# Kernel optimization log

Hardware: AMD Instinct MI355X
Metric: run time of the kernel (lower is better)

The kernel has to match this reference:

```python
import jax, jax.numpy as jnp
import numpy as np

N = 100000   # nodes
E = 1600000  # edges
H = 128      # hidden_dim
B = 4096     # number of root pairs
HOPS = 3


def setup_inputs() -> dict:
    key = jax.random.key(0)
    ks = jax.random.split(key, 12)
    s = 0.05
    return {
        "node_feat": jax.random.normal(ks[0], (N, H), jnp.float32),
        "send_embd": jax.random.normal(ks[1], (N, H), jnp.float32),
        "edge_index": jax.random.randint(ks[2], (2, E), 0, N, dtype=jnp.int32),
        "root_index": jax.random.randint(ks[3], (2 * B,), 0, N, dtype=jnp.int32),
        "agg_by_source": 1,
        "lin1_W": jax.random.normal(ks[4], (2 * H, H), jnp.float32) * s,
        "lin1_b": jnp.zeros((H,), jnp.float32),
        "gat_W": jax.random.normal(ks[5], (HOPS, H, H), jnp.float32) * s,
        "gat_asrc": jax.random.normal(ks[6], (HOPS, H), jnp.float32) * s,
        "gat_adst": jax.random.normal(ks[7], (HOPS, H), jnp.float32) * s,
        "gat_b": jnp.zeros((HOPS, H), jnp.float32),
        "lstm_Wih": jax.random.normal(ks[8], (HOPS, 2 * H, 4 * H), jnp.float32) * s,
        "lstm_Whh": jax.random.normal(ks[9], (HOPS, H, 4 * H), jnp.float32) * s,
        "lstm_b": jnp.zeros((HOPS, 4 * H), jnp.float32),
        "lin2_W": jax.random.normal(ks[10], (H, H), jnp.float32) * s,
        "lin2_b": jnp.zeros((H,), jnp.float32),
    }


def _gat_breadth(x, src, dst, W, a_src, a_dst, b):
    # GATConv(heads=1) followed by tanh (GeniePath Breadth layer)
    xw = x @ W                                  # [N, H]
    e_score = jax.nn.leaky_relu((xw @ a_src)[src] + (xw @ a_dst)[dst], 0.2)  # [E]
    # softmax over incoming edges of each destination node
    m = jax.ops.segment_max(e_score, dst, num_segments=N)
    ex = jnp.exp(e_score - m[dst])
    z = jax.ops.segment_sum(ex, dst, num_segments=N)
    alpha = ex / z[dst]                          # [E]
    agg = jax.ops.segment_sum(alpha[:, None] * xw[src], dst, num_segments=N)
    return jnp.tanh(agg + b)


def _lstm_step(inp, h, c, Wih, Whh, b):
    gates = inp @ Wih + h @ Whh + b              # [N, 4H]
    i, f, g, o = jnp.split(gates, 4, axis=-1)
    c = jax.nn.sigmoid(f) * c + jax.nn.sigmoid(i) * jnp.tanh(g)
    h = jax.nn.sigmoid(o) * jnp.tanh(c)
    return h, c


def reference(node_feat, send_embd, edge_index, root_index, agg_by_source,
              lin1_W, lin1_b, gat_W, gat_asrc, gat_adst, gat_b,
              lstm_Wih, lstm_Whh, lstm_b, lin2_W, lin2_b):
    src, dst = edge_index[0], edge_index[1]
    # Aggregation stage input: concat node embedding with broadcast embedding
    x = jnp.concatenate([node_feat, send_embd], axis=1) @ lin1_W + lin1_b  # [N, H]
    # GeniePathLazy: all breadth (GAT) layers run on the projected input x
    h_tmps = [
        _gat_breadth(x, src, dst, gat_W[i], gat_asrc[i], gat_adst[i], gat_b[i])
        for i in range(HOPS)
    ]
    # Depth: per-node LSTM over the hop axis, input = cat(h_tmp, x_prev)
    h = jnp.zeros_like(x)
    c = jnp.zeros_like(x)
    xs = x
    for i in range(HOPS):
        inp = jnp.concatenate([h_tmps[i], xs], axis=1)   # [N, 2H]
        h, c = _lstm_step(inp, h, c, lstm_Wih[i], lstm_Whh[i], lstm_b[i])
        xs = h
    out = xs @ lin2_W + lin2_b                            # [N, H]
    roots = root_index.reshape(-1, 2)
    src_nodes = roots[:, 0] if agg_by_source else roots[:, 1]
    return out[src_nodes]                                 # [B, H]
```

## Files before the change

kernel.cpp:

```cpp
#include <hip/hip_runtime.h>

constexpr int N  = 100000;
constexpr int E  = 1600000;
constexpr int H  = 128;
constexpr int NB = 4096;
constexpr int HOPS = 3;

constexpr int WOFF_L1  = 0;
constexpr int WOFF_GAT = 32768;
constexpr int WOFF_CAT = 81920;
constexpr int WOFF_L2  = 671744;
constexpr int WTOT     = 688128;

constexpr size_t ALIGN = 256;
constexpr size_t alup(size_t x) { return (x + ALIGN - 1) & ~(ALIGN - 1); }

constexpr size_t OFF_X       = 0;
constexpr size_t OFF_SSRC    = alup(OFF_X + (size_t)N * H * 4);
constexpr size_t OFF_SDST    = alup(OFF_SSRC + (size_t)3 * N * 4);
constexpr size_t OFF_WVEC    = alup(OFF_SDST + (size_t)3 * N * 4);
constexpr size_t OFF_SELMAP  = alup(OFF_WVEC + 6 * H * 4);
constexpr size_t OFF_NODELST = alup(OFF_SELMAP + (size_t)N * 4);
constexpr size_t OFF_CNT     = alup(OFF_NODELST + NB * 4);
constexpr size_t OFF_DEG     = alup(OFF_CNT + 256);
constexpr size_t OFF_OFFS    = alup(OFF_DEG + NB * 4);
constexpr size_t OFF_CURSOR  = alup(OFF_OFFS + (NB + 1) * 4);
constexpr size_t OFF_ESORT   = alup(OFF_CURSOR + NB * 4);
constexpr size_t OFF_AGGXH   = alup(OFF_ESORT + (size_t)E * 4);
constexpr size_t OFF_AGGXL   = alup(OFF_AGGXH + (size_t)3 * NB * H * 2);
constexpr size_t OFF_XSH     = alup(OFF_AGGXL + (size_t)3 * NB * H * 2);
constexpr size_t OFF_XSL     = alup(OFF_XSH + (size_t)NB * H * 2);
constexpr size_t OFF_HH      = alup(OFF_XSL + (size_t)NB * H * 2);
constexpr size_t OFF_HL      = alup(OFF_HH + (size_t)NB * H * 2);
constexpr size_t OFF_CBUF    = alup(OFF_HL + (size_t)NB * H * 2);
constexpr size_t OFF_L2OUT   = alup(OFF_CBUF + (size_t)NB * H * 4);
constexpr size_t OFF_WHI     = alup(OFF_L2OUT + (size_t)NB * H * 4);
constexpr size_t OFF_WLO     = alup(OFF_WHI + (size_t)WTOT * 2);

__device__ __forceinline__ float lrelu(float v) { return v > 0.f ? v : 0.2f * v; }
__device__ __forceinline__ float sigmoidf_(float v) { return 1.f / (1.f + __expf(-v)); }

__device__ __forceinline__ unsigned short f2bf(float f) {
  unsigned u = __float_as_uint(f);
  unsigned r = (u + 0x7FFFu + ((u >> 16) & 1u)) >> 16;
  return (unsigned short)r;
}
__device__ __forceinline__ float bf2f(unsigned short h) {
  return __uint_as_float((unsigned)h << 16);
}
__device__ __forceinline__ void split_rne(float f, unsigned short& hi, unsigned short& lo) {
// ... 4 lines not shown
__device__ __forceinline__ void split_trunc(float f, short* hi, short* lo) {
  unsigned u = __float_as_uint(f);
  *hi = (short)(u >> 16);
  float r = f - __uint_as_float(u & 0xFFFF0000u);
  *lo = (short)(__float_as_uint(r) >> 16);
}

typedef short bf16x8 __attribute__((ext_vector_type(8)));
typedef float f32x4  __attribute__((ext_vector_type(4)));

#define MFMA3(ACC, AH, AL, BH, BL)                                               \
  ACC = __builtin_amdgcn_mfma_f32_16x16x32_bf16(AH, BH, ACC, 0, 0, 0);           \
  ACC = __builtin_amdgcn_mfma_f32_16x16x32_bf16(AH, BL, ACC, 0, 0, 0);           \
  ACC = __builtin_amdgcn_mfma_f32_16x16x32_bf16(AL, BH, ACC, 0, 0, 0);

__global__ void init_ws(int* __restrict__ sel_map, int* __restrict__ deg,
                        int* __restrict__ cursor, int* __restrict__ cnt,
                        float* __restrict__ cbuf, unsigned short* __restrict__ hh,
                        unsigned short* __restrict__ hl) {
  int i = blockIdx.x * 256 + threadIdx.x;
  int stride = gridDim.x * 256;
  for (int n = i; n < N; n += stride) sel_map[n] = -1;
  for (int n = i; n < NB; n += stride) { deg[n] = 0; cursor[n] = 0; }
  if (i < 64) cnt[i] = 0;
  for (int n = i; n < NB * H; n += stride) { cbuf[n] = 0.f; hh[n] = 0; hl[n] = 0; }
}

__global__ void prep_kernel(const float* __restrict__ gat_W,
                            const float* __restrict__ a_src,
                            const float* __restrict__ a_dst,
                            float* __restrict__ wvec,
                            const float* __restrict__ lin1_W,
                            const float* __restrict__ Wih,
                            const float* __restrict__ Whh,
                            const float* __restrict__ lin2_W,
                            unsigned short* __restrict__ whi,
                            unsigned short* __restrict__ wlo) {
  if (blockIdx.x < 6) {
    int i = blockIdx.x >> 1, which = blockIdx.x & 1;
    int k = threadIdx.x;
    __shared__ float av[H];
    if (k < H) av[k] = which ? a_dst[i * H + k] : a_src[i * H + k];
    __syncthreads();
    if (k >= H) return;
    const float* Wr = gat_W + (size_t)i * H * H + (size_t)k * H;
    float s = 0.f;
    #pragma unroll 8
    for (int j = 0; j < H; j++) s = fmaf(Wr[j], av[j], s);
    wvec[(i * 2 + which) * H + k] = s;
    return;
  }
  int idx = (blockIdx.x - 6) * 256 + threadIdx.x;
  if (idx >= WTOT) return;
  float v;
  if (idx < WOFF_GAT) {
    int rel = idx;
    int e = rel & 7, lane = (rel >> 3) & 63, tile = rel >> 9;
    int nl = lane & 15, quad = lane >> 4;
    int c = tile & 7, t = tile >> 3;
    int n = c * 16 + nl, k = t * 32 + quad * 8 + e;
    v = lin1_W[k * 128 + n];
  } else if (idx < WOFF_CAT) {
    int rel = idx - WOFF_GAT;
    int hop = rel / 16384; rel %= 16384;
    int e = rel & 7, lane = (rel >> 3) & 63, tile = rel >> 9;
    int nl = lane & 15, quad = lane >> 4;
    int c = tile & 7, t = tile >> 3;
    int n = c * 16 + nl, k = t * 32 + quad * 8 + e;
    v = gat_W[hop * 16384 + k * 128 + n];
  } else if (idx < WOFF_L2) {
    int rel = idx - WOFF_CAT;
    int hop = rel / 196608; rel %= 196608;
    int e = rel & 7, lane = (rel >> 3) & 63, tile = rel >> 9;
    int nl = lane & 15, quad = lane >> 4;
    int c = tile & 31, t = tile >> 5;
    int ftile = c >> 2, g = c & 3;
    int col = g * 128 + ftile * 16 + nl;
    int k = t * 32 + quad * 8 + e;
    v = (k < 256) ? Wih[hop * 131072 + k * 512 + col]
                  : Whh[hop * 65536 + (k - 256) * 512 + col];
  } else {
    int rel = idx - WOFF_L2;
    int e = rel & 7, lane = (rel >> 3) & 63, tile = rel >> 9;
    int nl = lane & 15, quad = lane >> 4;
    int c = tile & 7, t = tile >> 3;
    int n = c * 16 + nl, k = t * 32 + quad * 8 + e;
    v = lin2_W[k * 128 + n];
  }
  unsigned short hh, ll;
  split_rne(v, hh, ll);
  whi[idx] = hh;
  wlo[idx] = ll;
}

__global__ void roots_assign(const int* __restrict__ root, const int* __restrict__ aggp,
                             int* __restrict__ sel_map, int* __restrict__ node_list,
                             int* __restrict__ cnt) {
  int b = blockIdx.x * 256 + threadIdx.x;
  if (b >= NB) return;
  int node = root[2 * b + (aggp[0] ? 0 : 1)];
  int old = atomicCAS(&sel_map[node], -1, -2);
  if (old == -1) {
    int c = atomicAdd(cnt, 1);
    sel_map[node] = c;
    node_list[c] = node;
  }
}

__global__ __launch_bounds__(256)
void gemm_lin1(const float* __restrict__ a0, const float* __restrict__ a1,
               const unsigned short* __restrict__ Bth,
               const unsigned short* __restrict__ Btl,
               const float* __restrict__ bias, float* __restrict__ Cc,
               const float* __restrict__ wvec,
               float* __restrict__ s_src, float* __restrict__ s_dst, int M) {
  const int t = threadIdx.x, lane = t & 63, wave = t >> 6;
  const int nl = lane & 15, quad = lane >> 4;
  const int rt = blockIdx.x * 128 + wave * 32;

  f32x4 acc[2][8];
  #pragma unroll
  for (int i = 0; i < 2; i++)
    #pragma unroll
    for (int c = 0; c < 8; c++) acc[i][c] = (f32x4){0.f, 0.f, 0.f, 0.f};

  #pragma unroll
  for (int kt = 0; kt < 8; kt++) {
    const float* A = (kt < 4) ? a0 : a1;
    const int kk = (kt & 3) * 32 + quad * 8;
    bf16x8 ahi[2], alo[2];
    #pragma unroll
    for (int i = 0; i < 2; i++) {
      int row = rt + i * 16 + nl;
      float4 v0 = make_float4(0.f, 0.f, 0.f, 0.f), v1 = v0;
      if (row < M) {
        const float* p = A + (size_t)row * H + kk;
        v0 = *(const float4*)p;
        v1 = *(const float4*)(p + 4);
      }
      float af[8] = {v0.x, v0.y, v0.z, v0.w, v1.x, v1.y, v1.z, v1.w};
      #pragma unroll
      for (int j = 0; j < 8; j++) {
        short h_, l_;
        split_trunc(af[j], &h_, &l_);
        ahi[i][j] = h_;
        alo[i][j] = l_;
      }
    }
    #pragma unroll
    for (int c = 0; c < 8; c++) {
      size_t boff = ((size_t)(kt * 8 + c) * 64 + lane) * 8;
      bf16x8 bh = *(const bf16x8*)(Bth + boff);
      bf16x8 bl = *(const bf16x8*)(Btl + boff);
      #pragma unroll
      for (int i = 0; i < 2; i++) { MFMA3(acc[i][c], ahi[i], alo[i], bh, bl); }
    }
  }

  float bv[8], wvf[6][8];
  #pragma unroll
  for (int c = 0; c < 8; c++) {
    int col = c * 16 + nl;
    bv[c] = bias[col];
    #pragma unroll
    for (int v6 = 0; v6 < 6; v6++) wvf[v6][c] = wvec[v6 * 128 + col];
  }
  #pragma unroll
  for (int i = 0; i < 2; i++)
    #pragma unroll
    for (int r = 0; r < 4; r++) {
      int row = rt + i * 16 + quad * 4 + r;
      if (row >= M) continue;
      float* cr = Cc + (size_t)row * H;
      float sc[6] = {0.f, 0.f, 0.f, 0.f, 0.f, 0.f};
      #pragma unroll
      for (int c = 0; c < 8; c++) {
        float val = acc[i][c][r] + bv[c];
        cr[c * 16 + nl] = val;
        #pragma unroll
        for (int v6 = 0; v6 < 6; v6++) sc[v6] = fmaf(val, wvf[v6][c], sc[v6]);
      }
      #pragma unroll
      for (int m = 1; m < 16; m <<= 1)
        #pragma unroll
        for (int v6 = 0; v6 < 6; v6++) sc[v6] += __shfl_xor(sc[v6], m);
      if (nl == 0) {
        #pragma unroll
        for (int h3 = 0; h3 < 3; h3++) {
          s_src[h3 * N + row] = sc[2 * h3 + 0];
          s_dst[h3 * N + row] = sc[2 * h3 + 1];
        }
      }
    }
}

__global__ void count_edges(const int* __restrict__ ei, const int* __restrict__ sel_map,
                            int* __restrict__ deg) {
  int e = blockIdx.x * 256 + threadIdx.x;
  if (e >= E) return;
  int d = sel_map[ei[E + e]];
  if (d >= 0) atomicAdd(&deg[d], 1);
}

__global__ __launch_bounds__(1024)
void scan_kernel(const int* __restrict__ deg, int* __restrict__ offs) {
  __shared__ int part[1024];
  int t = threadIdx.x;
  int base = t * 4;
  int v0 = deg[base], v1 = deg[base + 1], v2 = deg[base + 2], v3 = deg[base + 3];
  int s = v0 + v1 + v2 + v3;
  part[t] = s;
  __syncthreads();
  for (int off = 1; off < 1024; off <<= 1) {
    int tmp = (t >= off) ? part[t - off] : 0;
    __syncthreads();
    part[t] += tmp;
    __syncthreads();
  }
  int run = part[t] - s;
  offs[base] = run; run += v0;
  offs[base + 1] = run; run += v1;
  offs[base + 2] = run; run += v2;
  offs[base + 3] = run; run += v3;
  if (t == 1023) offs[NB] = part[1023];
}

__global__ void scatter_edges2(const int* __restrict__ ei, const int* __restrict__ sel_map,
                               const int* __restrict__ offs, int* __restrict__ cursor,
                               int* __restrict__ es_sorted) {
  int e = blockIdx.x * 256 + threadIdx.x;
  if (e >= E) return;
  int d = sel_map[ei[E + e]];
  if (d >= 0) {
    int p = atomicAdd(&cursor[d], 1);
    es_sorted[offs[d] + p] = ei[e];
  }
}

__global__ __launch_bounds__(128)
void gat_node_kernel(const int* __restrict__ node_list, const int* __restrict__ cntp,
                     const int* __restrict__ offs, const int* __restrict__ es_sorted,
                     const float* __restrict__ x, const float* __restrict__ s_src,
                     const float* __restrict__ s_dst,
                     unsigned short* __restrict__ aggxh, unsigned short* __restrict__ aggxl,
                     unsigned short* __restrict__ xsh, unsigned short* __restrict__ xsl) {
  int c = blockIdx.x;
  if (c >= cntp[0]) return;
  int t = threadIdx.x;
  int n = node_list[c];
  {
    float xv = x[(size_t)n * H + t];
    unsigned short vh, vl;
    split_rne(xv, vh, vl);
    xsh[(size_t)c * H + t] = vh;
    xsl[(size_t)c * H + t] = vl;
  }
  float sd0 = s_dst[0 * N + n], sd1 = s_dst[1 * N + n], sd2 = s_dst[2 * N + n];
  int e0 = offs[c], e1 = offs[c + 1];
  float m0 = -1e30f, m1 = -1e30f, m2 = -1e30f;
  for (int e = e0 + t; e < e1; e += 128) {
    int s = es_sorted[e];
    m0 = fmaxf(m0, lrelu(s_src[0 * N + s] + sd0));
    m1 = fmaxf(m1, lrelu(s_src[1 * N + s] + sd1));
    m2 = fmaxf(m2, lrelu(s_src[2 * N + s] + sd2));
  }
  __shared__ float red[3][128];
  red[0][t] = m0; red[1][t] = m1; red[2][t] = m2;
  __syncthreads();
  for (int s2 = 64; s2 > 0; s2 >>= 1) {
    if (t < s2) {
      red[0][t] = fmaxf(red[0][t], red[0][t + s2]);
      red[1][t] = fmaxf(red[1][t], red[1][t + s2]);
      red[2][t] = fmaxf(red[2][t], red[2][t + s2]);
    }
    __syncthreads();
  }
  m0 = red[0][0]; m1 = red[1][0]; m2 = red[2][0];
  float u0 = 0.f, u1 = 0.f, u2 = 0.f, z0 = 0.f, z1 = 0.f, z2 = 0.f;
  for (int e = e0; e < e1; e++) {
    int s = es_sorted[e];
    float xs = x[(size_t)s * H + t];
    float ex0 = __expf(lrelu(s_src[0 * N + s] + sd0) - m0);
    float ex1 = __expf(lrelu(s_src[1 * N + s] + sd1) - m1);
    float ex2 = __expf(lrelu(s_src[2 * N + s] + sd2) - m2);
    z0 += ex0; z1 += ex1; z2 += ex2;
    u0 = fmaf(ex0, xs, u0); u1 = fmaf(ex1, xs, u1); u2 = fmaf(ex2, xs, u2);
  }
  size_t cb = (size_t)c * H + t;
  bool any = e1 > e0;
  float v0 = any ? u0 / z0 : 0.f;
  float v1 = any ? u1 / z1 : 0.f;
  float v2 = any ? u2 / z2 : 0.f;
  unsigned short vh, vl;
  split_rne(v0, vh, vl); aggxh[0 * ((size_t)NB * H) + cb] = vh; aggxl[0 * ((size_t)NB * H) + cb] = vl;
  split_rne(v1, vh, vl); aggxh[1 * ((size_t)NB * H) + cb] = vh; aggxl[1 * ((size_t)NB * H) + cb] = vl;
  split_rne(v2, vh, vl); aggxh[2 * ((size_t)NB * H) + cb] = vh; aggxl[2 * ((size_t)NB * H) + cb] = vl;
}

__global__ __launch_bounds__(256)
void hop_fused(const unsigned short* __restrict__ agh, const unsigned short* __restrict__ agl,
               const unsigned short* __restrict__ gWh, const unsigned short* __restrict__ gWl,
               const float* __restrict__ gbias,
               const unsigned short* __restrict__ x1h, const unsigned short* __restrict__ x1l,
               const unsigned short* __restrict__ CWh, const unsigned short* __restrict__ CWl,
               const float* __restrict__ lbias,
               float* __restrict__ cbuf, unsigned short* __restrict__ hh,
               unsigned short* __restrict__ hl,
               const unsigned short* __restrict__ L2h, const unsigned short* __restrict__ L2l,
               const float* __restrict__ lin2_b, float* __restrict__ l2out, int do_lin2) {
  __shared__ unsigned short Hh[16 * 136];
  __shared__ unsigned short Hl[16 * 136];
  const int t = threadIdx.x, lane = t & 63, wave = t >> 6;
  const int nl = lane & 15, quad = lane >> 4;
  const int r0 = blockIdx.x * 16;

  f32x4 acc1[2];
  #pragma unroll
  for (int j = 0; j < 2; j++) acc1[j] = (f32x4){0.f, 0.f, 0.f, 0.f};
  #pragma unroll
  for (int kt = 0; kt < 4; kt++) {
    size_t aoff = (size_t)(r0 + nl) * H + kt * 32 + quad * 8;
    bf16x8 ah = *(const bf16x8*)(agh + aoff);
    bf16x8 al = *(const bf16x8*)(agl + aoff);
    #pragma unroll
    for (int j = 0; j < 2; j++) {
      size_t boff = ((size_t)(kt * 8 + 2 * wave + j) * 64 + lane) * 8;
      bf16x8 bh = *(const bf16x8*)(gWh + boff);
      bf16x8 bl = *(const bf16x8*)(gWl + boff);
      MFMA3(acc1[j], ah, al, bh, bl);
    }
  }
  #pragma unroll
  for (int j = 0; j < 2; j++) {
    int col = wave * 32 + j * 16 + nl;
    float bv = gbias[col];
    #pragma unroll
    for (int r = 0; r < 4; r++) {
      int rl = quad * 4 + r;
      float v = tanhf(acc1[j][r] + bv);
      unsigned short vh, vl2;
      split_rne(v, vh, vl2);
      Hh[rl * 136 + col] = vh;
      Hl[rl * 136 + col] = vl2;
    }
  }
  __syncthreads();

  f32x4 acc2[8];
  #pragma unroll
  for (int j = 0; j < 8; j++) acc2[j] = (f32x4){0.f, 0.f, 0.f, 0.f};
  for (int kt = 0; kt < 12; kt++) {
    int kk = (kt & 3) * 32 + quad * 8;
    bf16x8 ah, al;
    if (kt < 4) {
      ah = *(const bf16x8*)&Hh[nl * 136 + kk];
      al = *(const bf16x8*)&Hl[nl * 136 + kk];
    } else {
      const unsigned short* ph = (kt < 8) ? x1h : hh;
      const unsigned short* pl = (kt < 8) ? x1l : hl;
      size_t aoff = (size_t)(r0 + nl) * H + kk;
      ah = *(const bf16x8*)(ph + aoff);
      al = *(const bf16x8*)(pl + aoff);
    }
    #pragma unroll
    for (int cc = 0; cc < 8; cc++) {
      size_t boff = ((size_t)(kt * 32 + 8 * wave + cc) * 64 + lane) * 8;
      bf16x8 bh = *(const bf16x8*)(CWh + boff);
      bf16x8 bl = *(const bf16x8*)(CWl + boff);
      MFMA3(acc2[cc], ah, al, bh, bl);
    }
  }
  __syncthreads();

  #pragma unroll
  for (int ft = 0; ft < 2; ft++) {
    int f = (2 * wave + ft) * 16 + nl;
    float b_i = lbias[0 * 128 + f], b_f = lbias[1 * 128 + f];
    float b_g = lbias[2 * 128 + f], b_o = lbias[3 * 128 + f];
    #pragma unroll
    for (int r = 0; r < 4; r++) {
      int rl = quad * 4 + r;
      size_t id = (size_t)(r0 + rl) * H + f;
      float gi = acc2[ft * 4 + 0][r] + b_i;
      float gf = acc2[ft * 4 + 1][r] + b_f;
      float gg = acc2[ft * 4 + 2][r] + b_g;
      float go = acc2[ft * 4 + 3][r] + b_o;
      float cp = cbuf[id];
      float cn = sigmoidf_(gf) * cp + sigmoidf_(gi) * tanhf(gg);
      float hn = sigmoidf_(go) * tanhf(cn);
      cbuf[id] = cn;
      unsigned short vh, vl2;
      split_rne(hn, vh, vl2);
      hh[id] = vh;
      hl[id] = vl2;
      if (do_lin2) { Hh[rl * 136 + f] = vh; Hl[rl * 136 + f] = vl2; }
    }
  }

  if (!do_lin2) return;
  __syncthreads();
  f32x4 acc3[2];
  #pragma unroll
  for (int j = 0; j < 2; j++) acc3[j] = (f32x4){0.f, 0.f, 0.f, 0.f};
  #pragma unroll
  for (int kt = 0; kt < 4; kt++) {
    int kk = kt * 32 + quad * 8;
    bf16x8 ah = *(const bf16x8*)&Hh[nl * 136 + kk];
    bf16x8 al = *(const bf16x8*)&Hl[nl * 136 + kk];
    #pragma unroll
    for (int j = 0; j < 2; j++) {
      size_t boff = ((size_t)(kt * 8 + 2 * wave + j) * 64 + lane) * 8;
      bf16x8 bh = *(const bf16x8*)(L2h + boff);
      bf16x8 bl = *(const bf16x8*)(L2l + boff);
      MFMA3(acc3[j], ah, al, bh, bl);
    }
  }
  #pragma unroll
  for (int j = 0; j < 2; j++) {
    int col = wave * 32 + j * 16 + nl;
    float bv = lin2_b[col];
    #pragma unroll
    for (int r = 0; r < 4; r++) {
      int row = r0 + quad * 4 + r;
      l2out[(size_t)row * H + col] = acc3[j][r] + bv;
    }
  }
}

// ... 18 lines not shown
  const int*   aggp      = (const int*)d_in[4];
  const float* lin1_W    = (const float*)d_in[5];
  const float* lin1_b    = (const float*)d_in[6];
  const float* gat_W     = (const float*)d_in[7];
  const float* gat_asrc  = (const float*)d_in[8];
  const float* gat_adst  = (const float*)d_in[9];
  const float* gat_b     = (const float*)d_in[10];
  const float* lstm_Wih  = (const float*)d_in[11];
  const float* lstm_Whh  = (const float*)d_in[12];
  const float* lstm_b    = (const float*)d_in[13];
  const float* lin2_W    = (const float*)d_in[14];
  const float* lin2_b    = (const float*)d_in[15];
  float* out = (float*)d_out;

  char* ws = (char*)d_ws;
  float* x       = (float*)(ws + OFF_X);
  float* s_src   = (float*)(ws + OFF_SSRC);
  float* s_dst   = (float*)(ws + OFF_SDST);
  float* wvec    = (float*)(ws + OFF_WVEC);
  int*   sel_map = (int*)(ws + OFF_SELMAP);
  int*   nodelst = (int*)(ws + OFF_NODELST);
  int*   cnt     = (int*)(ws + OFF_CNT);
  int*   deg     = (int*)(ws + OFF_DEG);
  int*   offs    = (int*)(ws + OFF_OFFS);
  int*   cursor  = (int*)(ws + OFF_CURSOR);
  int*   esort   = (int*)(ws + OFF_ESORT);
  unsigned short* aggxh = (unsigned short*)(ws + OFF_AGGXH);
  unsigned short* aggxl = (unsigned short*)(ws + OFF_AGGXL);
  unsigned short* xsh   = (unsigned short*)(ws + OFF_XSH);
  unsigned short* xsl   = (unsigned short*)(ws + OFF_XSL);
  unsigned short* hh    = (unsigned short*)(ws + OFF_HH);
  unsigned short* hl    = (unsigned short*)(ws + OFF_HL);
  float* cbuf    = (float*)(ws + OFF_CBUF);
  float* l2out   = (float*)(ws + OFF_L2OUT);
  unsigned short* whi = (unsigned short*)(ws + OFF_WHI);
  unsigned short* wlo = (unsigned short*)(ws + OFF_WLO);

  init_ws<<<2048, 256, 0, stream>>>(sel_map, deg, cursor, cnt, cbuf, hh, hl);
  prep_kernel<<<6 + (WTOT + 255) / 256, 256, 0, stream>>>(
      gat_W, gat_asrc, gat_adst, wvec, lin1_W, lstm_Wih, lstm_Whh, lin2_W, whi, wlo);
  roots_assign<<<(NB + 255) / 256, 256, 0, stream>>>(root_idx, aggp, sel_map, nodelst, cnt);

  gemm_lin1<<<(N + 127) / 128, 256, 0, stream>>>(
      node_feat, send_embd, whi + WOFF_L1, wlo + WOFF_L1, lin1_b, x,
      wvec, s_src, s_dst, N);

  count_edges<<<(E + 255) / 256, 256, 0, stream>>>(edge_idx, sel_map, deg);
  scan_kernel<<<1, 1024, 0, stream>>>(deg, offs);
  scatter_edges2<<<(E + 255) / 256, 256, 0, stream>>>(edge_idx, sel_map, offs, cursor, esort);
  gat_node_kernel<<<NB, 128, 0, stream>>>(nodelst, cnt, offs, esort, x, s_src, s_dst,
                                          aggxh, aggxl, xsh, xsl);

  for (int i = 0; i < HOPS; i++) {
    const unsigned short* x1h = (i == 0) ? xsh : hh;
    const unsigned short* x1l = (i == 0) ? xsl : hl;
    hop_fused<<<NB / 16, 256, 0, stream>>>(
        aggxh + (size_t)i * NB * H, aggxl + (size_t)i * NB * H,
        whi + WOFF_GAT + i * 16384, wlo + WOFF_GAT + i * 16384,
        gat_b + (size_t)i * H,
        x1h, x1l,
        whi + WOFF_CAT + i * 196608, wlo + WOFF_CAT + i * 196608,
        lstm_b + (size_t)i * 512,
        cbuf, hh, hl,
        whi + WOFF_L2, wlo + WOFF_L2, lin2_b, l2out,
        (i == HOPS - 1) ? 1 : 0);
  }

  scatter_out<<<(NB * H + 255) / 256, 256, 0, stream>>>(l2out, sel_map, root_idx, aggp, out);
}
```

Baseline: 377.2 us.

## Compute lin1 only for needed nodes and fuse hops into one kernel

The lin1 projection and attention scores are now computed only for rows that are roots or sources of edges into roots. These rows are collected through a needed flag and a compacted row list, with capacity RCAP. Several small kernels are merged: init goes into the prep kernel, and edge counting shares a kernel with the last-block scan. The three per-hop launches become one hop_all kernel that keeps the LSTM state in shared memory and drops the global cbuf/hh/hl buffers. Risks are a fixed capacity bound on needed rows and extra atomic and compaction work.

```diff
diff --git a/kernel.cpp b/kernel.cpp
--- a/kernel.cpp
+++ b/kernel.cpp
@@ -5,23 +5,28 @@
 constexpr int H  = 128;
 constexpr int NB = 4096;
 constexpr int HOPS = 3;
+constexpr int RCAP = 596 * 128;
 
 constexpr int WOFF_L1  = 0;
 constexpr int WOFF_GAT = 32768;
 constexpr int WOFF_CAT = 81920;
 constexpr int WOFF_L2  = 671744;
 constexpr int WTOT     = 688128;
+constexpr int WCONV_BLOCKS = (WTOT + 255) / 256;
 
 constexpr size_t ALIGN = 256;
 constexpr size_t alup(size_t x) { return (x + ALIGN - 1) & ~(ALIGN - 1); }
 
-constexpr size_t OFF_X       = 0;
-constexpr size_t OFF_SSRC    = alup(OFF_X + (size_t)N * H * 4);
-constexpr size_t OFF_SDST    = alup(OFF_SSRC + (size_t)3 * N * 4);
-constexpr size_t OFF_WVEC    = alup(OFF_SDST + (size_t)3 * N * 4);
+constexpr size_t OFF_XP      = 0;
+constexpr size_t OFF_SSRC    = alup(OFF_XP + (size_t)RCAP * H * 4);
+constexpr size_t OFF_SDST    = alup(OFF_SSRC + (size_t)3 * RCAP * 4);
+constexpr size_t OFF_WVEC    = alup(OFF_SDST + (size_t)3 * RCAP * 4);
 constexpr size_t OFF_SELMAP  = alup(OFF_WVEC + 6 * H * 4);
-constexpr size_t OFF_NODELST = alup(OFF_SELMAP + (size_t)N * 4);
-constexpr size_t OFF_CNT     = alup(OFF_NODELST + NB * 4);
+constexpr size_t OFF_NEEDED  = alup(OFF_SELMAP + (size_t)N * 4);
+constexpr size_t OFF_ROWID   = alup(OFF_NEEDED + (size_t)N * 4);
+constexpr size_t OFF_NODELST = alup(OFF_ROWID + (size_t)N * 4);
+constexpr size_t OFF_ROWLST  = alup(OFF_NODELST + NB * 4);
+constexpr size_t OFF_CNT     = alup(OFF_ROWLST + (size_t)RCAP * 4);
 constexpr size_t OFF_DEG     = alup(OFF_CNT + 256);
 constexpr size_t OFF_OFFS    = alup(OFF_DEG + NB * 4);
 constexpr size_t OFF_CURSOR  = alup(OFF_OFFS + (NB + 1) * 4);
@@ -30,10 +35,7 @@
 constexpr size_t OFF_AGGXL   = alup(OFF_AGGXH + (size_t)3 * NB * H * 2);
 constexpr size_t OFF_XSH     = alup(OFF_AGGXL + (size_t)3 * NB * H * 2);
 constexpr size_t OFF_XSL     = alup(OFF_XSH + (size_t)NB * H * 2);
-constexpr size_t OFF_HH      = alup(OFF_XSL + (size_t)NB * H * 2);
-constexpr size_t OFF_HL      = alup(OFF_HH + (size_t)NB * H * 2);
-constexpr size_t OFF_CBUF    = alup(OFF_HL + (size_t)NB * H * 2);
-constexpr size_t OFF_L2OUT   = alup(OFF_CBUF + (size_t)NB * H * 4);
+constexpr size_t OFF_L2OUT   = alup(OFF_XSL + (size_t)NB * H * 2);
 constexpr size_t OFF_WHI     = alup(OFF_L2OUT + (size_t)NB * H * 4);
 constexpr size_t OFF_WLO     = alup(OFF_WHI + (size_t)WTOT * 2);
 
@@ -68,28 +70,19 @@
   ACC = __builtin_amdgcn_mfma_f32_16x16x32_bf16(AH, BL, ACC, 0, 0, 0);           \
   ACC = __builtin_amdgcn_mfma_f32_16x16x32_bf16(AL, BH, ACC, 0, 0, 0);
 
-__global__ void init_ws(int* __restrict__ sel_map, int* __restrict__ deg,
-                        int* __restrict__ cursor, int* __restrict__ cnt,
-                        float* __restrict__ cbuf, unsigned short* __restrict__ hh,
-                        unsigned short* __restrict__ hl) {
-  int i = blockIdx.x * 256 + threadIdx.x;
-  int stride = gridDim.x * 256;
-  for (int n = i; n < N; n += stride) sel_map[n] = -1;
-  for (int n = i; n < NB; n += stride) { deg[n] = 0; cursor[n] = 0; }
-  if (i < 64) cnt[i] = 0;
-  for (int n = i; n < NB * H; n += stride) { cbuf[n] = 0.f; hh[n] = 0; hl[n] = 0; }
-}
-
-__global__ void prep_kernel(const float* __restrict__ gat_W,
-                            const float* __restrict__ a_src,
-                            const float* __restrict__ a_dst,
-                            float* __restrict__ wvec,
-                            const float* __restrict__ lin1_W,
-                            const float* __restrict__ Wih,
-                            const float* __restrict__ Whh,
-                            const float* __restrict__ lin2_W,
-                            unsigned short* __restrict__ whi,
-                            unsigned short* __restrict__ wlo) {
+__global__ void mega_prep(const float* __restrict__ gat_W,
+                          const float* __restrict__ a_src,
+                          const float* __restrict__ a_dst,
+                          float* __restrict__ wvec,
+                          const float* __restrict__ lin1_W,
+                          const float* __restrict__ Wih,
+                          const float* __restrict__ Whh,
+                          const float* __restrict__ lin2_W,
+                          unsigned short* __restrict__ whi,
+                          unsigned short* __restrict__ wlo,
+                          int* __restrict__ sel_map, int* __restrict__ needed,
+                          int* __restrict__ deg, int* __restrict__ cursor,
+                          int* __restrict__ cnt) {
   if (blockIdx.x < 6) {
     int i = blockIdx.x >> 1, which = blockIdx.x & 1;
     int k = threadIdx.x;
@@ -104,60 +97,133 @@
     wvec[(i * 2 + which) * H + k] = s;
     return;
   }
-  int idx = (blockIdx.x - 6) * 256 + threadIdx.x;
-  if (idx >= WTOT) return;
-  float v;
-  if (idx < WOFF_GAT) {
-    int rel = idx;
-    int e = rel & 7, lane = (rel >> 3) & 63, tile = rel >> 9;
-    int nl = lane & 15, quad = lane >> 4;
-    int c = tile & 7, t = tile >> 3;
-    int n = c * 16 + nl, k = t * 32 + quad * 8 + e;
-    v = lin1_W[k * 128 + n];
-  } else if (idx < WOFF_CAT) {
-    int rel = idx - WOFF_GAT;
-    int hop = rel / 16384; rel %= 16384;
-    int e = rel & 7, lane = (rel >> 3) & 63, tile = rel >> 9;
-    int nl = lane & 15, quad = lane >> 4;
-    int c = tile & 7, t = tile >> 3;
-    int n = c * 16 + nl, k = t * 32 + quad * 8 + e;
-    v = gat_W[hop * 16384 + k * 128 + n];
-  } else if (idx < WOFF_L2) {
-    int rel = idx - WOFF_CAT;
-    int hop = rel / 196608; rel %= 196608;
-    int e = rel & 7, lane = (rel >> 3) & 63, tile = rel >> 9;
-    int nl = lane & 15, quad = lane >> 4;
-    int c = tile & 31, t = tile >> 5;
-    int ftile = c >> 2, g = c & 3;
-    int col = g * 128 + ftile * 16 + nl;
-    int k = t * 32 + quad * 8 + e;
-    v = (k < 256) ? Wih[hop * 131072 + k * 512 + col]
-                  : Whh[hop * 65536 + (k - 256) * 512 + col];
-  } else {
-    int rel = idx - WOFF_L2;
-    int e = rel & 7, lane = (rel >> 3) & 63, tile = rel >> 9;
-    int nl = lane & 15, quad = lane >> 4;
-    int c = tile & 7, t = tile >> 3;
-    int n = c * 16 + nl, k = t * 32 + quad * 8 + e;
-    v = lin2_W[k * 128 + n];
-  }
-  unsigned short hh, ll;
-  split_rne(v, hh, ll);
-  whi[idx] = hh;
-  wlo[idx] = ll;
+  if (blockIdx.x < 6 + WCONV_BLOCKS) {
+    int idx = (blockIdx.x - 6) * 256 + threadIdx.x;
+    if (idx >= WTOT) return;
+    float v;
+    if (idx < WOFF_GAT) {
+      int rel = idx;
+      int e = rel & 7, lane = (rel >> 3) & 63, tile = rel >> 9;
+      int nl = lane & 15, quad = lane >> 4;
+      int c = tile & 7, t = tile >> 3;
+      int n = c * 16 + nl, k = t * 32 + quad * 8 + e;
+      v = lin1_W[k * 128 + n];
+    } else if (idx < WOFF_CAT) {
+      int rel = idx - WOFF_GAT;
+      int hop = rel / 16384; rel %= 16384;
+      int e = rel & 7, lane = (rel >> 3) & 63, tile = rel >> 9;
+      int nl = lane & 15, quad = lane >> 4;
+      int c = tile & 7, t = tile >> 3;
+      int n = c * 16 + nl, k = t * 32 + quad * 8 + e;
+      v = gat_W[hop * 16384 + k * 128 + n];
+    } else if (idx < WOFF_L2) {
+      int rel = idx - WOFF_CAT;
+      int hop = rel / 196608; rel %= 196608;
+      int e = rel & 7, lane = (rel >> 3) & 63, tile = rel >> 9;
+      int nl = lane & 15, quad = lane >> 4;
+      int c = tile & 31, t = tile >> 5;
+      int ftile = c >> 2, g = c & 3;
+      int col = g * 128 + ftile * 16 + nl;
+      int k = t * 32 + quad * 8 + e;
+      v = (k < 256) ? Wih[hop * 131072 + k * 512 + col]
+                    : Whh[hop * 65536 + (k - 256) * 512 + col];
+    } else {
+      int rel = idx - WOFF_L2;
+      int e = rel & 7, lane = (rel >> 3) & 63, tile = rel >> 9;
+      int nl = lane & 15, quad = lane >> 4;
+      int c = tile & 7, t = tile >> 3;
+      int n = c * 16 + nl, k = t * 32 + quad * 8 + e;
+      v = lin2_W[k * 128 + n];
+    }
+    unsigned short hh, ll;
+    split_rne(v, hh, ll);
+    whi[idx] = hh;
+    wlo[idx] = ll;
+    return;
+  }
+  int i = (blockIdx.x - 6 - WCONV_BLOCKS) * 256 + threadIdx.x;
+  int stride = 256 * 256;
+  for (int n = i; n < N; n += stride) { sel_map[n] = -1; needed[n] = 0; }
+  for (int n = i; n < NB; n += stride) { deg[n] = 0; cursor[n] = 0; }
+  if (i < 64) cnt[i] = 0;
 }
 
 __global__ void roots_assign(const int* __restrict__ root, const int* __restrict__ aggp,
                              int* __restrict__ sel_map, int* __restrict__ node_list,
-                             int* __restrict__ cnt) {
+                             int* __restrict__ cnt, int* __restrict__ needed) {
   int b = blockIdx.x * 256 + threadIdx.x;
   if (b >= NB) return;
   int node = root[2 * b + (aggp[0] ? 0 : 1)];
+  needed[node] = 1;
   int old = atomicCAS(&sel_map[node], -1, -2);
   if (old == -1) {
-    int c = atomicAdd(cnt, 1);
+    int c = atomicAdd(&cnt[0], 1);
     sel_map[node] = c;
     node_list[c] = node;
+  }
+}
+
+__global__ void count_scan(const int* __restrict__ ei, const int* __restrict__ sel_map,
+                           int* __restrict__ deg, int* __restrict__ needed,
+                           int* __restrict__ cnt, int* __restrict__ offs) {
+  int e = blockIdx.x * 256 + threadIdx.x;
+  if (e < E) {
+    int d = sel_map[ei[E + e]];
+    if (d >= 0) {
+      atomicAdd(&deg[d], 1);
+      needed[ei[e]] = 1;
+    }
+  }
+  __shared__ int islast;
+  __syncthreads();
+  if (threadIdx.x == 0) {
+    __threadfence();
+    islast = (atomicAdd(&cnt[2], 1) == (int)gridDim.x - 1) ? 1 : 0;
+  }
+  __syncthreads();
+  if (!islast) return;
+  __shared__ int psum[256];
+  int tid = threadIdx.x;
+  int base = tid * 16;
+  int loc[16];
+  int s = 0;
+  #pragma unroll
+  for (int j = 0; j < 16; j++) { loc[j] = atomicAdd(&deg[base + j], 0); s += loc[j]; }
+  psum[tid] = s;
+  __syncthreads();
+  for (int off = 1; off < 256; off <<= 1) {
+    int tmp = (tid >= off) ? psum[tid - off] : 0;
+    __syncthreads();
+    psum[tid] += tmp;
+    __syncthreads();
+  }
+  int run = psum[tid] - s;
+  #pragma unroll
+  for (int j = 0; j < 16; j++) { offs[base + j] = run; run += loc[j]; }
+  if (tid == 255) offs[NB] = run;
+}
+
+__global__ void scatter_rows(const int* __restrict__ ei, const int* __restrict__ sel_map,
+                             const int* __restrict__ offs, int* __restrict__ cursor,
+                             int* __restrict__ es_sorted,
+                             const int* __restrict__ needed, int* __restrict__ rowid,
+                             int* __restrict__ rowlist, int* __restrict__ cnt) {
+  if (blockIdx.x < (E + 255) / 256) {
+    int e = blockIdx.x * 256 + threadIdx.x;
+    if (e >= E) return;
+    int d = sel_map[ei[E + e]];
+    if (d >= 0) {
+      int p = atomicAdd(&cursor[d], 1);
+      es_sorted[offs[d] + p] = ei[e];
+    }
+  } else {
+    int n = (blockIdx.x - (E + 255) / 256) * 256 + threadIdx.x;
+    if (n >= N) return;
+    if (needed[n]) {
+      int r = atomicAdd(&cnt[1], 1);
+      rowid[n] = r;
+      rowlist[r] = n;
+    }
   }
 }
 
@@ -165,50 +231,75 @@
 void gemm_lin1(const float* __restrict__ a0, const float* __restrict__ a1,
                const unsigned short* __restrict__ Bth,
                const unsigned short* __restrict__ Btl,
-               const float* __restrict__ bias, float* __restrict__ Cc,
+               const float* __restrict__ bias, float* __restrict__ xp,
                const float* __restrict__ wvec,
-               float* __restrict__ s_src, float* __restrict__ s_dst, int M) {
+               float* __restrict__ s_src, float* __restrict__ s_dst,
+               const int* __restrict__ rowlist, const int* __restrict__ cnt) {
+  __shared__ unsigned short BsH[8192];
+  __shared__ unsigned short BsL[8192];
+  const int rcnt = cnt[1];
+  if (blockIdx.x * 128 >= rcnt) return;
   const int t = threadIdx.x, lane = t & 63, wave = t >> 6;
   const int nl = lane & 15, quad = lane >> 4;
   const int rt = blockIdx.x * 128 + wave * 32;
 
+  int node[2];
+  #pragma unroll
+  for (int i = 0; i < 2; i++) {
+    int r = rt + i * 16 + nl;
+    node[i] = (r < rcnt) ? rowlist[r] : -1;
+  }
+
   f32x4 acc[2][8];
   #pragma unroll
   for (int i = 0; i < 2; i++)
     #pragma unroll
     for (int c = 0; c < 8; c++) acc[i][c] = (f32x4){0.f, 0.f, 0.f, 0.f};
 
-  #pragma unroll
-  for (int kt = 0; kt < 8; kt++) {
-    const float* A = (kt < 4) ? a0 : a1;
-    const int kk = (kt & 3) * 32 + quad * 8;
-    bf16x8 ahi[2], alo[2];
-    #pragma unroll
-    for (int i = 0; i < 2; i++) {
-      int row = rt + i * 16 + nl;
-      float4 v0 = make_float4(0.f, 0.f, 0.f, 0.f), v1 = v0;
-      if (row < M) {
-        const float* p = A + (size_t)row * H + kk;
-        v0 = *(const float4*)p;
-        v1 = *(const float4*)(p + 4);
-      }
-      float af[8] = {v0.x, v0.y, v0.z, v0.w, v1.x, v1.y, v1.z, v1.w};
-      #pragma unroll
-      for (int j = 0; j < 8; j++) {
-        short h_, l_;
-        split_trunc(af[j], &h_, &l_);
-        ahi[i][j] = h_;
-        alo[i][j] = l_;
-      }
-    }
-    #pragma unroll
-    for (int c = 0; c < 8; c++) {
-      size_t boff = ((size_t)(kt * 8 + c) * 64 + lane) * 8;
-      bf16x8 bh = *(const bf16x8*)(Bth + boff);
-      bf16x8 bl = *(const bf16x8*)(Btl + boff);
-      #pragma unroll
-      for (int i = 0; i < 2; i++) { MFMA3(acc[i][c], ahi[i], alo[i], bh, bl); }
-    }
+  for (int st = 0; st < 4; st++) {
+    {
+      int sb = st * 8192;
+      #pragma unroll
+      for (int u = 0; u < 4; u++) {
+        int o = (u * 256 + t) * 8;
+        *(bf16x8*)&BsH[o] = *(const bf16x8*)(Bth + sb + o);
+        *(bf16x8*)&BsL[o] = *(const bf16x8*)(Btl + sb + o);
+      }
+    }
+    __syncthreads();
+    #pragma unroll
+    for (int u = 0; u < 2; u++) {
+      const int kt = st * 2 + u;
+      const float* A = (kt < 4) ? a0 : a1;
+      const int kk = (kt & 3) * 32 + quad * 8;
+      bf16x8 ahi[2], alo[2];
+      #pragma unroll
+      for (int i = 0; i < 2; i++) {
+        float4 v0 = make_float4(0.f, 0.f, 0.f, 0.f), v1 = v0;
+        if (node[i] >= 0) {
+          const float* p = A + (size_t)node[i] * H + kk;
+          v0 = *(const float4*)p;
+          v1 = *(const float4*)(p + 4);
+        }
+        float af[8] = {v0.x, v0.y, v0.z, v0.w, v1.x, v1.y, v1.z, v1.w};
+        #pragma unroll
+        for (int j = 0; j < 8; j++) {
+          short h_, l_;
+          split_trunc(af[j], &h_, &l_);
+          ahi[i][j] = h_;
+          alo[i][j] = l_;
+        }
+      }
+      #pragma unroll
+      for (int c = 0; c < 8; c++) {
+        int off = ((u * 8 + c) * 64 + lane) * 8;
+        bf16x8 bh = *(const bf16x8*)&BsH[off];
+        bf16x8 bl = *(const bf16x8*)&BsL[off];
+        #pragma unroll
+        for (int i = 0; i < 2; i++) { MFMA3(acc[i][c], ahi[i], alo[i], bh, bl); }
+      }
+    }
+    __syncthreads();
   }
 
   float bv[8], wvf[6][8];
@@ -224,8 +315,8 @@
     #pragma unroll
     for (int r = 0; r < 4; r++) {
       int row = rt + i * 16 + quad * 4 + r;
-      if (row >= M) continue;
-      float* cr = Cc + (size_t)row * H;
+      if (row >= rcnt) continue;
+      float* cr = xp + (size_t)row * H;
       float sc[6] = {0.f, 0.f, 0.f, 0.f, 0.f, 0.f};
       #pragma unroll
       for (int c = 0; c < 8; c++) {
@@ -241,104 +332,57 @@
       if (nl == 0) {
         #pragma unroll
         for (int h3 = 0; h3 < 3; h3++) {
-          s_src[h3 * N + row] = sc[2 * h3 + 0];
-          s_dst[h3 * N + row] = sc[2 * h3 + 1];
+          s_src[h3 * RCAP + row] = sc[2 * h3 + 0];
+          s_dst[h3 * RCAP + row] = sc[2 * h3 + 1];
         }
       }
     }
 }
 
-__global__ void count_edges(const int* __restrict__ ei, const int* __restrict__ sel_map,
-                            int* __restrict__ deg) {
-  int e = blockIdx.x * 256 + threadIdx.x;
-  if (e >= E) return;
-  int d = sel_map[ei[E + e]];
-  if (d >= 0) atomicAdd(&deg[d], 1);
-}
-
-__global__ __launch_bounds__(1024)
-void scan_kernel(const int* __restrict__ deg, int* __restrict__ offs) {
-  __shared__ int part[1024];
-  int t = threadIdx.x;
-  int base = t * 4;
-  int v0 = deg[base], v1 = deg[base + 1], v2 = deg[base + 2], v3 = deg[base + 3];
-  int s = v0 + v1 + v2 + v3;
-  part[t] = s;
-  __syncthreads();
-  for (int off = 1; off < 1024; off <<= 1) {
-    int tmp = (t >= off) ? part[t - off] : 0;
-    __syncthreads();
-    part[t] += tmp;
-    __syncthreads();
-  }
-  int run = part[t] - s;
-  offs[base] = run; run += v0;
-  offs[base + 1] = run; run += v1;
-  offs[base + 2] = run; run += v2;
-  offs[base + 3] = run; run += v3;
-  if (t == 1023) offs[NB] = part[1023];
-}
-
-__global__ void scatter_edges2(const int* __restrict__ ei, const int* __restrict__ sel_map,
-                               const int* __restrict__ offs, int* __restrict__ cursor,
-                               int* __restrict__ es_sorted) {
-  int e = blockIdx.x * 256 + threadIdx.x;
-  if (e >= E) return;
-  int d = sel_map[ei[E + e]];
-  if (d >= 0) {
-    int p = atomicAdd(&cursor[d], 1);
-    es_sorted[offs[d] + p] = ei[e];
-  }
-}
-
 __global__ __launch_bounds__(128)
-void gat_node_kernel(const int* __restrict__ node_list, const int* __restrict__ cntp,
+void gat_node_kernel(const int* __restrict__ node_list, const int* __restrict__ cnt,
                      const int* __restrict__ offs, const int* __restrict__ es_sorted,
-                     const float* __restrict__ x, const float* __restrict__ s_src,
+                     const int* __restrict__ rowid,
+                     const float* __restrict__ xp, const float* __restrict__ s_src,
                      const float* __restrict__ s_dst,
                      unsigned short* __restrict__ aggxh, unsigned short* __restrict__ aggxl,
                      unsigned short* __restrict__ xsh, unsigned short* __restrict__ xsl) {
   int c = blockIdx.x;
-  if (c >= cntp[0]) return;
+  if (c >= cnt[0]) return;
   int t = threadIdx.x;
   int n = node_list[c];
+  int rn = rowid[n];
   {
-    float xv = x[(size_t)n * H + t];
+    float xv = xp[(size_t)rn * H + t];
     unsigned short vh, vl;
     split_rne(xv, vh, vl);
     xsh[(size_t)c * H + t] = vh;
     xsl[(size_t)c * H + t] = vl;
   }
-  float sd0 = s_dst[0 * N + n], sd1 = s_dst[1 * N + n], sd2 = s_dst[2 * N + n];
+  float sd0 = s_dst[0 * RCAP + rn], sd1 = s_dst[1 * RCAP + rn], sd2 = s_dst[2 * RCAP + rn];
   int e0 = offs[c], e1 = offs[c + 1];
-  float m0 = -1e30f, m1 = -1e30f, m2 = -1e30f;
-  for (int e = e0 + t; e < e1; e += 128) {
-    int s = es_sorted[e];
-    m0 = fmaxf(m0, lrelu(s_src[0 * N + s] + sd0));
-    m1 = fmaxf(m1, lrelu(s_src[1 * N + s] + sd1));
-    m2 = fmaxf(m2, lrelu(s_src[2 * N + s] + sd2));
-  }
-  __shared__ float red[3][128];
-  red[0][t] = m0; red[1][t] = m1; red[2][t] = m2;
-  __syncthreads();
-  for (int s2 = 64; s2 > 0; s2 >>= 1) {
-    if (t < s2) {
-      red[0][t] = fmaxf(red[0][t], red[0][t + s2]);
-      red[1][t] = fmaxf(red[1][t], red[1][t + s2]);
-      red[2][t] = fmaxf(red[2][t], red[2][t + s2]);
-    }
-    __syncthreads();
-  }
-  m0 = red[0][0]; m1 = red[1][0]; m2 = red[2][0];
+  __shared__ float exs[3][128];
+  __shared__ int rss[128];
   float u0 = 0.f, u1 = 0.f, u2 = 0.f, z0 = 0.f, z1 = 0.f, z2 = 0.f;
-  for (int e = e0; e < e1; e++) {
-    int s = es_sorted[e];
-    float xs = x[(size_t)s * H + t];
-    float ex0 = __expf(lrelu(s_src[0 * N + s] + sd0) - m0);
-    float ex1 = __expf(lrelu(s_src[1 * N + s] + sd1) - m1);
-    float ex2 = __expf(lrelu(s_src[2 * N + s] + sd2) - m2);
-    z0 += ex0; z1 += ex1; z2 += ex2;
-    u0 = fmaf(ex0, xs, u0); u1 = fmaf(ex1, xs, u1); u2 = fmaf(ex2, xs, u2);
+  for (int base = e0; base < e1; base += 128) {
+    int e = base + t;
+    if (e < e1) {
+      int s = es_sorted[e];
+      int rs = rowid[s];
+      rss[t] = rs;
+      exs[0][t] = __expf(lrelu(s_src[0 * RCAP + rs] + sd0));
+      exs[1][t] = __expf(lrelu(s_src[1 * RCAP + rs] + sd1));
+      exs[2][t] = __expf(lrelu(s_src[2 * RCAP + rs] + sd2));
+    }
+    __syncthreads();
+    int m = min(128, e1 - base);
+    for (int j = 0; j < m; j++) {
+      float xs = xp[(size_t)rss[j] * H + t];
+      float ex0 = exs[0][j], ex1 = exs[1][j], ex2 = exs[2][j];
+      z0 += ex0; z1 += ex1; z2 += ex2;
+      u0 = fmaf(ex0, xs, u0); u1 = fmaf(ex1, xs, u1); u2 = fmaf(ex2, xs, u2);
+    }
+    __syncthreads();
   }
   size_t cb = (size_t)c * H + t;
   bool any = e1 > e0;
@@ -352,120 +396,129 @@
 }
 
 __global__ __launch_bounds__(256)
-void hop_fused(const unsigned short* __restrict__ agh, const unsigned short* __restrict__ agl,
-               const unsigned short* __restrict__ gWh, const unsigned short* __restrict__ gWl,
-               const float* __restrict__ gbias,
-               const unsigned short* __restrict__ x1h, const unsigned short* __restrict__ x1l,
-               const unsigned short* __restrict__ CWh, const unsigned short* __restrict__ CWl,
-               const float* __restrict__ lbias,
-               float* __restrict__ cbuf, unsigned short* __restrict__ hh,
-               unsigned short* __restrict__ hl,
-               const unsigned short* __restrict__ L2h, const unsigned short* __restrict__ L2l,
-               const float* __restrict__ lin2_b, float* __restrict__ l2out, int do_lin2) {
-  __shared__ unsigned short Hh[16 * 136];
-  __shared__ unsigned short Hl[16 * 136];
+void hop_all(const unsigned short* __restrict__ aggxh, const unsigned short* __restrict__ aggxl,
+             const unsigned short* __restrict__ xsh, const unsigned short* __restrict__ xsl,
+             const unsigned short* __restrict__ whi, const unsigned short* __restrict__ wlo,
+             const float* __restrict__ gat_b, const float* __restrict__ lstm_b,
+             const float* __restrict__ lin2_b, float* __restrict__ l2out) {
+  __shared__ unsigned short HtH[16 * 136], HtL[16 * 136];
+  __shared__ unsigned short HsH[16 * 136], HsL[16 * 136];
+  __shared__ float Cst[16 * 128];
   const int t = threadIdx.x, lane = t & 63, wave = t >> 6;
   const int nl = lane & 15, quad = lane >> 4;
   const int r0 = blockIdx.x * 16;
 
-  f32x4 acc1[2];
-  #pragma unroll
-  for (int j = 0; j < 2; j++) acc1[j] = (f32x4){0.f, 0.f, 0.f, 0.f};
+  for (int i = t; i < 16 * 136; i += 256) { HsH[i] = 0; HsL[i] = 0; }
+  for (int i = t; i < 16 * 128; i += 256) Cst[i] = 0.f;
+  __syncthreads();
+
+  for (int hop = 0; hop < HOPS; hop++) {
+    const unsigned short* agh = aggxh + (size_t)hop * NB * H;
+    const unsigned short* agl = aggxl + (size_t)hop * NB * H;
+    const unsigned short* gWh = whi + WOFF_GAT + hop * 16384;
+    const unsigned short* gWl = wlo + WOFF_GAT + hop * 16384;
+    const unsigned short* CWh = whi + WOFF_CAT + hop * 196608;
+    const unsigned short* CWl = wlo + WOFF_CAT + hop * 196608;
+    const float* gbias = gat_b + hop * H;
+    const float* lbias = lstm_b + hop * 512;
+
+    f32x4 acc1[2];
+    #pragma unroll
+    for (int j = 0; j < 2; j++) acc1[j] = (f32x4){0.f, 0.f, 0.f, 0.f};
+    #pragma unroll
+    for (int kt = 0; kt < 4; kt++) {
+      size_t aoff = (size_t)(r0 + nl) * H + kt * 32 + quad * 8;
+      bf16x8 ah = *(const bf16x8*)(agh + aoff);
+      bf16x8 al = *(const bf16x8*)(agl + aoff);
+      #pragma unroll
+      for (int j = 0; j < 2; j++) {
+        size_t boff = ((size_t)(kt * 8 + 2 * wave + j) * 64 + lane) * 8;
+        bf16x8 bh = *(const bf16x8*)(gWh + boff);
+        bf16x8 bl = *(const bf16x8*)(gWl + boff);
+        MFMA3(acc1[j], ah, al, bh, bl);
+      }
+    }
+    #pragma unroll
+    for (int j = 0; j < 2; j++) {
+      int col = wave * 32 + j * 16 + nl;
+      float bv = gbias[col];
+      #pragma unroll
+      for (int r = 0; r < 4; r++) {
+        int rl = quad * 4 + r;
+        float v = tanhf(acc1[j][r] + bv);
+        unsigned short vh, vl2;
+        split_rne(v, vh, vl2);
+        HtH[rl * 136 + col] = vh;
+        HtL[rl * 136 + col] = vl2;
+      }
+    }
+    __syncthreads();
+
+    f32x4 acc2[8];
+    #pragma unroll
+    for (int j = 0; j < 8; j++) acc2[j] = (f32x4){0.f, 0.f, 0.f, 0.f};
+    for (int kt = 0; kt < 12; kt++) {
+      int kk = (kt & 3) * 32 + quad * 8;
+      bf16x8 ah, al;
+      if (kt < 4) {
+        ah = *(const bf16x8*)&HtH[nl * 136 + kk];
+        al = *(const bf16x8*)&HtL[nl * 136 + kk];
+      } else if (kt < 8 && hop == 0) {
+        size_t aoff = (size_t)(r0 + nl) * H + kk;
+        ah = *(const bf16x8*)(xsh + aoff);
+        al = *(const bf16x8*)(xsl + aoff);
+      } else {
+        ah = *(const bf16x8*)&HsH[nl * 136 + kk];
+        al = *(const bf16x8*)&HsL[nl * 136 + kk];
+      }
+      #pragma unroll
+      for (int cc = 0; cc < 8; cc++) {
+        size_t boff = ((size_t)(kt * 32 + 8 * wave + cc) * 64 + lane) * 8;
+        bf16x8 bh = *(const bf16x8*)(CWh + boff);
+        bf16x8 bl = *(const bf16x8*)(CWl + boff);
+        MFMA3(acc2[cc], ah, al, bh, bl);
+      }
+    }
+    __syncthreads();
+
+    #pragma unroll
+    for (int ft = 0; ft < 2; ft++) {
+      int f = (2 * wave + ft) * 16 + nl;
+      float b_i = lbias[0 * 128 + f], b_f = lbias[1 * 128 + f];
+      float b_g = lbias[2 * 128 + f], b_o = lbias[3 * 128 + f];
+      #pragma unroll
+      for (int r = 0; r < 4; r++) {
+        int rl = quad * 4 + r;
+        float gi = acc2[ft * 4 + 0][r] + b_i;
+        float gf = acc2[ft * 4 + 1][r] + b_f;
+        float gg = acc2[ft * 4 + 2][r] + b_g;
+        float go = acc2[ft * 4 + 3][r] + b_o;
+        float cp = Cst[rl * 128 + f];
+        float cn = sigmoidf_(gf) * cp + sigmoidf_(gi) * tanhf(gg);
+        float hn = sigmoidf_(go) * tanhf(cn);
+        Cst[rl * 128 + f] = cn;
+        unsigned short vh, vl2;
+        split_rne(hn, vh, vl2);
+        HsH[rl * 136 + f] = vh;
+        HsL[rl * 136 + f] = vl2;
+      }
+    }
+    __syncthreads();
+  }
+
+  f32x4 acc3[2];
+  #pragma unroll
+  for (int j = 0; j < 2; j++) acc3[j] = (f32x4){0.f, 0.f, 0.f, 0.f};
   #pragma unroll
   for (int kt = 0; kt < 4; kt++) {
-    size_t aoff = (size_t)(r0 + nl) * H + kt * 32 + quad * 8;
-    bf16x8 ah = *(const bf16x8*)(agh + aoff);
-    bf16x8 al = *(const bf16x8*)(agl + aoff);
+    int kk = kt * 32 + quad * 8;
+    bf16x8 ah = *(const bf16x8*)&HsH[nl * 136 + kk];
+    bf16x8 al = *(const bf16x8*)&HsL[nl * 136 + kk];
     #pragma unroll
     for (int j = 0; j < 2; j++) {
       size_t boff = ((size_t)(kt * 8 + 2 * wave + j) * 64 + lane) * 8;
-      bf16x8 bh = *(const bf16x8*)(gWh + boff);
-      bf16x8 bl = *(const bf16x8*)(gWl + boff);
-      MFMA3(acc1[j], ah, al, bh, bl);
-    }
-  }
-  #pragma unroll
-  for (int j = 0; j < 2; j++) {
-    int col = wave * 32 + j * 16 + nl;
-    float bv = gbias[col];
-    #pragma unroll
-    for (int r = 0; r < 4; r++) {
-      int rl = quad * 4 + r;
-      float v = tanhf(acc1[j][r] + bv);
-      unsigned short vh, vl2;
-      split_rne(v, vh, vl2);
-      Hh[rl * 136 + col] = vh;
-      Hl[rl * 136 + col] = vl2;
-    }
-  }
-  __syncthreads();
-
-  f32x4 acc2[8];
-  #pragma unroll
-  for (int j = 0; j < 8; j++) acc2[j] = (f32x4){0.f, 0.f, 0.f, 0.f};
-  for (int kt = 0; kt < 12; kt++) {
-    int kk = (kt & 3) * 32 + quad * 8;
-    bf16x8 ah, al;
-    if (kt < 4) {
-      ah = *(const bf16x8*)&Hh[nl * 136 + kk];
-      al = *(const bf16x8*)&Hl[nl * 136 + kk];
-    } else {
-      const unsigned short* ph = (kt < 8) ? x1h : hh;
-      const unsigned short* pl = (kt < 8) ? x1l : hl;
-      size_t aoff = (size_t)(r0 + nl) * H + kk;
-      ah = *(const bf16x8*)(ph + aoff);
-      al = *(const bf16x8*)(pl + aoff);
-    }
-    #pragma unroll
-    for (int cc = 0; cc < 8; cc++) {
-      size_t boff = ((size_t)(kt * 32 + 8 * wave + cc) * 64 + lane) * 8;
-      bf16x8 bh = *(const bf16x8*)(CWh + boff);
-      bf16x8 bl = *(const bf16x8*)(CWl + boff);
-      MFMA3(acc2[cc], ah, al, bh, bl);
-    }
-  }
-  __syncthreads();
-
-  #pragma unroll
-  for (int ft = 0; ft < 2; ft++) {
-    int f = (2 * wave + ft) * 16 + nl;
-    float b_i = lbias[0 * 128 + f], b_f = lbias[1 * 128 + f];
-    float b_g = lbias[2 * 128 + f], b_o = lbias[3 * 128 + f];
-    #pragma unroll
-    for (int r = 0; r < 4; r++) {
-      int rl = quad * 4 + r;
-      size_t id = (size_t)(r0 + rl) * H + f;
-      float gi = acc2[ft * 4 + 0][r] + b_i;
-      float gf = acc2[ft * 4 + 1][r] + b_f;
-      float gg = acc2[ft * 4 + 2][r] + b_g;
-      float go = acc2[ft * 4 + 3][r] + b_o;
-      float cp = cbuf[id];
-      float cn = sigmoidf_(gf) * cp + sigmoidf_(gi) * tanhf(gg);
-      float hn = sigmoidf_(go) * tanhf(cn);
-      cbuf[id] = cn;
-      unsigned short vh, vl2;
-      split_rne(hn, vh, vl2);
-      hh[id] = vh;
-      hl[id] = vl2;
-      if (do_lin2) { Hh[rl * 136 + f] = vh; Hl[rl * 136 + f] = vl2; }
-    }
-  }
-
-  if (!do_lin2) return;
-  __syncthreads();
-  f32x4 acc3[2];
-  #pragma unroll
-  for (int j = 0; j < 2; j++) acc3[j] = (f32x4){0.f, 0.f, 0.f, 0.f};
-  #pragma unroll
-  for (int kt = 0; kt < 4; kt++) {
-    int kk = kt * 32 + quad * 8;
-    bf16x8 ah = *(const bf16x8*)&Hh[nl * 136 + kk];
-    bf16x8 al = *(const bf16x8*)&Hl[nl * 136 + kk];
-    #pragma unroll
-    for (int j = 0; j < 2; j++) {
-      size_t boff = ((size_t)(kt * 8 + 2 * wave + j) * 64 + lane) * 8;
-      bf16x8 bh = *(const bf16x8*)(L2h + boff);
-      bf16x8 bl = *(const bf16x8*)(L2l + boff);
+      bf16x8 bh = *(const bf16x8*)(whi + WOFF_L2 + boff);
+      bf16x8 bl = *(const bf16x8*)(wlo + WOFF_L2 + boff);
       MFMA3(acc3[j], ah, al, bh, bl);
     }
   }
@@ -514,12 +567,15 @@
   float* out = (float*)d_out;
 
   char* ws = (char*)d_ws;
-  float* x       = (float*)(ws + OFF_X);
+  float* xp      = (float*)(ws + OFF_XP);
   float* s_src   = (float*)(ws + OFF_SSRC);
   float* s_dst   = (float*)(ws + OFF_SDST);
   float* wvec    = (float*)(ws + OFF_WVEC);
   int*   sel_map = (int*)(ws + OFF_SELMAP);
+  int*   needed  = (int*)(ws + OFF_NEEDED);
+  int*   rowid   = (int*)(ws + OFF_ROWID);
   int*   nodelst = (int*)(ws + OFF_NODELST);
+  int*   rowlst  = (int*)(ws + OFF_ROWLST);
   int*   cnt     = (int*)(ws + OFF_CNT);
   int*   deg     = (int*)(ws + OFF_DEG);
   int*   offs    = (int*)(ws + OFF_OFFS);
@@ -529,42 +585,28 @@
   unsigned short* aggxl = (unsigned short*)(ws + OFF_AGGXL);
   unsigned short* xsh   = (unsigned short*)(ws + OFF_XSH);
   unsigned short* xsl   = (unsigned short*)(ws + OFF_XSL);
-  unsigned short* hh    = (unsigned short*)(ws + OFF_HH);
-  unsigned short* hl    = (unsigned short*)(ws + OFF_HL);
-  float* cbuf    = (float*)(ws + OFF_CBUF);
   float* l2out   = (float*)(ws + OFF_L2OUT);
   unsigned short* whi = (unsigned short*)(ws + OFF_WHI);
   unsigned short* wlo = (unsigned short*)(ws + OFF_WLO);
 
-  init_ws<<<2048, 256, 0, stream>>>(sel_map, deg, cursor, cnt, cbuf, hh, hl);
-  prep_kernel<<<6 + (WTOT + 255) / 256, 256, 0, stream>>>(
-      gat_W, gat_asrc, gat_adst, wvec, lin1_W, lstm_Wih, lstm_Whh, lin2_W, whi, wlo);
-  roots_assign<<<(NB + 255) / 256, 256, 0, stream>>>(root_idx, aggp, sel_map, nodelst, cnt);
-
-  gemm_lin1<<<(N + 127) / 128, 256, 0, stream>>>(
-      node_feat, send_embd, whi + WOFF_L1, wlo + WOFF_L1, lin1_b, x,
-      wvec, s_src, s_dst, N);
-
-  count_edges<<<(E + 255) / 256, 256, 0, stream>>>(edge_idx, sel_map, deg);
-  scan_kernel<<<1, 1024, 0, stream>>>(deg, offs);
-  scatter_edges2<<<(E + 255) / 256, 256, 0, stream>>>(edge_idx, sel_map, offs, cursor, esort);
-  gat_node_kernel<<<NB, 128, 0, stream>>>(nodelst, cnt, offs, esort, x, s_src, s_dst,
-                                          aggxh, aggxl, xsh, xsl);
-
-  for (int i = 0; i < HOPS; i++) {
-    const unsigned short* x1h = (i == 0) ? xsh : hh;
-    const unsigned short* x1l = (i == 0) ? xsl : hl;
-    hop_fused<<<NB / 16, 256, 0, stream>>>(
-        aggxh + (size_t)i * NB * H, aggxl + (size_t)i * NB * H,
-        whi + WOFF_GAT + i * 16384, wlo + WOFF_GAT + i * 16384,
-        gat_b + (size_t)i * H,
-        x1h, x1l,
-        whi + WOFF_CAT + i * 196608, wlo + WOFF_CAT + i * 196608,
-        lstm_b + (size_t)i * 512,
-        cbuf, hh, hl,
-        whi + WOFF_L2, wlo + WOFF_L2, lin2_b, l2out,
-        (i == HOPS - 1) ? 1 : 0);
-  }
-
-  scatter_out<<<(NB * H + 255) / 256, 256, 0, stream>>>(l2out, sel_map, root_idx, aggp, out);
-}
+  const int EB = (E + 255) / 256;
+  const int NBK = (N + 255) / 256;
+
+  mega_prep<<<6 + WCONV_BLOCKS + 256, 256, 0, stream>>>(
+      gat_W, gat_asrc, gat_adst, wvec, lin1_W, lstm_Wih, lstm_Whh, lin2_W,
+      whi, wlo, sel_map, needed, deg, cursor, cnt);
+  roots_assign<<<(NB + 255) / 256, 256, 0, stream>>>(root_idx, aggp, sel_map,
+                                                     nodelst, cnt, needed);
+  count_scan<<<EB, 256, 0, stream>>>(edge_idx, sel_map, deg, needed, cnt, offs);
+  scatter_rows<<<EB + NBK, 256, 0, stream>>>(edge_idx, sel_map, offs, cursor, esort,
+                                             needed, rowid, rowlst, cnt);
+  gemm_lin1<<<RCAP / 128, 256, 0, stream>>>(
+      node_feat, send_embd, whi + WOFF_L1, wlo + WOFF_L1, lin1_b, xp,
+      wvec, s_src, s_dst, rowlst, cnt);
+  gat_node_kernel<<<NB, 128, 0, stream>>>(nodelst, cnt, offs, esort, rowid,
+                                          xp, s_src, s_dst, aggxh, aggxl, xsh, xsl);
+  hop_all<<<NB / 16, 256, 0, stream>>>(aggxh, aggxl, xsh, xsl, whi, wlo,
+                                       gat_b, lstm_b, lin2_b, l2out);
+  scatter_out<<<(NB * H + 255) / 256, 256, 0, stream>>>(l2out, sel_map, root_idx,
+                                                        aggp, out);
+}
```

Measured after the change: 504.1 us. 1.34x slower.
